# Optimization experiments

Measured on AMD Instinct MI355X. Metric: run time of the kernel, lower is better.

Reference implementation:

```python
import jax, jax.numpy as jnp
import numpy as np

EPS = 1e-30
NEG = -1e30  # finite stand-in for -inf (safe under vjp, exp underflows to 0)


def _build_tree(L):
    """Perfect binary tree with L leaves (L power of 2) plus a unifurcating root.
    Node ids are level-contiguous (leaves first), which is a valid postorder-compatible
    numbering for the level-synchronous pruning loop."""
    depth = int(np.log2(L))
    total = 2 * L  # (2L-1) perfect-tree nodes + 1 unifurcating root
    children = np.full((total, 2), -1, dtype=np.int64)
    parents = np.full(total, -1, dtype=np.int64)
    levels = np.zeros(total, dtype=np.int64)
    offs = np.zeros(depth + 1, dtype=np.int64)
    for h in range(1, depth + 1):
        offs[h] = offs[h - 1] + (L >> (h - 1))
    for h in range(1, depth + 1):
        n = L >> h
        ids = offs[h] + np.arange(n)
        lkid = offs[h - 1] + 2 * np.arange(n)
        children[ids, 0] = lkid
        children[ids, 1] = lkid + 1
        parents[lkid] = ids
        parents[lkid + 1] = ids
        levels[ids] = h
    root = total - 1
    top = offs[depth]  # the single node at level `depth`
    children[root, 0] = top  # unifurcating root: right child = -1
    parents[top] = root
    levels[root] = depth + 1
    return children, parents, levels


def setup_inputs() -> dict:
    key = jax.random.key(0)
    S = 16
    L = 32768  # leaves -> N = 65536 nodes
    children, parents, levels = _build_tree(L)
    N = children.shape[0]
    postorder = np.arange(N, dtype=np.int64)
    k1, k2, k3, k4 = jax.random.split(key, 4)
    branch_lens = jax.random.uniform(k1, (N,), jnp.float32, 0.05, 0.5)
    branch_lens = branch_lens.at[N - 1].set(0.0)  # root edge has length 0
    # CTMC-style rate matrix: nonneg off-diagonals, rows sum to 0
    off = jax.random.uniform(k2, (S, S), jnp.float32, 0.1, 1.0) * (1.0 - jnp.eye(S, dtype=jnp.float32))
    Q = off - jnp.diag(off.sum(axis=1))
    growth_rates = jax.random.uniform(k3, (S,), jnp.float32, 0.5, 1.5)
    leaf_states = np.asarray(jax.random.randint(k4, (L,), 0, S))
    init_partials = np.full((N, S), NEG, dtype=np.float32)
    init_partials[np.arange(L), leaf_states] = 0.0  # leaf one-hots in log space
    return {
        "postorder": jnp.asarray(postorder),
        "children": jnp.asarray(children),
        "parents": jnp.asarray(parents),
        "branch_lens": branch_lens,
        "init_partials": jnp.asarray(init_partials),
        "Q": Q,
        "levels": jnp.asarray(levels),
        "growth_rates": growth_rates,
    }


def _log_prune(branch_lens, init_partials, Q, growth_rates, po, ch, lv):
    S = Q.shape[0]
    # rho == 1.0 path of FelsensteinPruner.log_prune
    rate = Q - jnp.diag(growth_rates)
    scaled = rate[None, :, :] * branch_lens[:, None, None]      # (N, S, S)
    trans = jax.vmap(jax.scipy.linalg.expm)(scaled)             # batched matrix_exp
    I = jnp.eye(S, dtype=Q.dtype)
    trans = jnp.where((branch_lens <= EPS)[:, None, None], I[None], trans)
    log_trans = jnp.log(jnp.clip(trans, EPS))
    log_growth = jnp.log(growth_rates)
    log_partials = init_partials
    max_level = int(lv.max())
    for lvl in range(1, max_level + 1):  # tree topology is static -> static level groups
        node_idxs = po[lv == lvl]
        left = ch[node_idxs, 0]
        right = ch[node_idxs, 1]
        # left_contrib[n, p] = logsumexp_c( log P_left[n, p, c] + L_left[n, c] )
        lc = jax.nn.logsumexp(log_trans[left] + log_partials[left][:, None, :], axis=2)
        valid = np.nonzero(right >= 0)[0]
        rc = jnp.zeros_like(lc)
        if valid.size > 0:
            rv = right[valid]
            rc_v = jax.nn.logsumexp(log_trans[rv] + log_partials[rv][:, None, :], axis=2)
            rc_v = rc_v + log_growth[None, :]  # growth_rates term on the right child
            rc = rc.at[valid].set(rc_v)
        log_partials = log_partials.at[node_idxs].set(lc + rc)
    root = int(po[lv == max_level][0])
    return log_partials[root]


def reference(postorder, children, parents, branch_lens, init_partials, Q, levels, growth_rates):
    po = np.asarray(postorder)
    ch = np.asarray(children)
    lv = np.asarray(levels)
    return _log_prune(branch_lens, init_partials, Q, growth_rates, po, ch, lv)
```

## Files before the change

### kernel.cpp

```cpp
#include <hip/hip_runtime.h>
#include <math.h>

#define KORD 10
#define NC   (KORD + 1)
#define NTOT 65536
#define MAGIC 0x5A17C0DEu

typedef float f32x2 __attribute__((ext_vector_type(2)));

static constexpr int WS_U6  = 0;
static constexpr int WS_S6  = 8192;
static constexpr int WS_U11 = 8704;
static constexpr int WS_S11 = 8960;
static constexpr int WS_F1  = 8976;
static constexpr int WS_F2  = 9488;


template <int CTRL>
__device__ __forceinline__ float qperm_add(float x) {
  const int xi = __builtin_bit_cast(int, x);
  const int yi = __builtin_amdgcn_mov_dpp(xi, CTRL, 0xF, 0xF, true);
  return x + __builtin_bit_cast(float, yi);
}

__device__ __forceinline__ float horner_dot(const f32x2* c01, const f32x2* c23,
                                            float tv, float4 uu) {
  const f32x2 t2 = {tv, tv};
  f32x2 a01 = c01[KORD], a23 = c23[KORD];
  #pragma unroll
  for (int k = KORD - 1; k >= 0; --k) {
    a01 = __builtin_elementwise_fma(a01, t2, c01[k]);
    a23 = __builtin_elementwise_fma(a23, t2, c23[k]);
  }
  const f32x2 u01 = {uu.x, uu.y}, u23 = {uu.z, uu.w};
  f32x2 mm = a01 * u01;
  mm = __builtin_elementwise_fma(a23, u23, mm);
  float yy = mm.x + mm.y;
  yy = qperm_add<0xB1>(yy);
  yy = qperm_add<0x4E>(yy);
  return yy;
}

__device__ __forceinline__ int tree_sweep(
    float* ubuf, float* sbuf, const float* blB,
    const f32x2* c01, const f32x2* c23, float sigma, float gp,
    int IN, int depth, int t)
{
  const int lane = t & 63;
  const int wid = t >> 6;
  const int p = (lane >> 2) & 15;
  const int q = lane & 3;
  int off_in = 0, bloff = 0;
  for (int ll = 1; ll <= depth; ++ll) {
    const int cnt = IN >> ll;
    const int off_out = off_in + (IN >> (ll - 1));
    for (int n = wid; n < cnt; n += 8) {
      const int cl = 2 * n, cr = cl + 1;
      const float tl = blB[bloff + cl];
      const float tr = blB[bloff + cr];
      const float4 uL = *(const float4*)&ubuf[(off_in + cl) * 16 + q * 4];
      const float4 uR = *(const float4*)&ubuf[(off_in + cr) * 16 + q * 4];
      const float yl = horner_dot(c01, c23, tl, uL);
      const float yr = horner_dot(c01, c23, tr, uR);
      const float val = yl * yr * gp;
      const float mx = __shfl(val, 28 + q, 64);
      const float un = val * __builtin_amdgcn_rcpf(mx);
      if (q == 0) ubuf[(off_out + n) * 16 + p] = un;
      if (lane == 0)
        sbuf[off_out + n] = sbuf[off_in + cl] + sbuf[off_in + cr] +
                            sigma * (tl + tr) + __logf(mx);
    }
    bloff += IN >> (ll - 1);
    off_in = off_out;
    __syncthreads();
  }
  return off_in;
}

__device__ __forceinline__ void stage_bl(float* blB, const float* bl,
                                         int b, int IN, int depth,
                                         int level_in, int tt) {
  int loff = 0;
  for (int ll = 1; ll <= depth; ++ll) {
    const int cnt_c = IN >> (ll - 1);
    const int gl = level_in + ll - 1;
    const int cbase = (gl == 0) ? 0 : (NTOT - (NTOT >> gl));
    if (tt < cnt_c) blB[loff + tt] = bl[cbase + b * cnt_c + tt];
    loff += cnt_c;
  }
}

__device__ __forceinline__ void poll_reset(unsigned int* f) {
  while (__hip_atomic_load(f, __ATOMIC_RELAXED, __HIP_MEMORY_SCOPE_AGENT)
         != MAGIC)
    __builtin_amdgcn_s_sleep(1);
  __hip_atomic_store(f, 0u, __ATOMIC_RELAXED, __HIP_MEMORY_SCOPE_AGENT);
}

__device__ __forceinline__ float row_dot16(const float4* row, const float* col) {
  const float4 r0 = row[0], r1 = row[1], r2 = row[2], r3 = row[3];
  float s = r0.x * col[0];
  s = fmaf(r0.y, col[1], s);  s = fmaf(r0.z, col[2], s);
  s = fmaf(r0.w, col[3], s);  s = fmaf(r1.x, col[4], s);
  s = fmaf(r1.y, col[5], s);  s = fmaf(r1.z, col[6], s);
  s = fmaf(r1.w, col[7], s);  s = fmaf(r2.x, col[8], s);
  s = fmaf(r2.y, col[9], s);  s = fmaf(r2.z, col[10], s);
  s = fmaf(r2.w, col[11], s); s = fmaf(r3.x, col[12], s);
  s = fmaf(r3.y, col[13], s); s = fmaf(r3.z, col[14], s);
  s = fmaf(r3.w, col[15], s);
  return s;
}

__global__ __launch_bounds__(512) void k_all(
    const float* __restrict__ bl, const float* __restrict__ init_p,
    const float* __restrict__ Q, const float* __restrict__ g,
    float* __restrict__ ws, float* __restrict__ out)
{
  __shared__ __align__(16) float Bs[256];
  __shared__ __align__(16) float BsT[256];
  __shared__ __align__(16) float B2T[256];
  __shared__ __align__(16) float Cs[NC * 256];
  __shared__ __align__(16) float ubuf[127 * 16];
  __shared__ float sbuf[127];
  __shared__ float blB[128];
  __shared__ float sdiag[16];
  __shared__ float s_sig;

  const int t = threadIdx.x, b = blockIdx.x;
  const int lane = t & 63, wid = t >> 6;
  const int p = (lane >> 2) & 15, q = lane & 3;
  const int i = (t & 255) >> 4, j = t & 15;
  unsigned int* f1 = (unsigned int*)(ws + WS_F1);
  unsigned int* f2 = (unsigned int*)(ws + WS_F2);

  float4 leafv;
  float blr[6];
  const int tt = t - 256;
  if (t >= 256) {
    leafv = ((const float4*)init_p)[b * 256 + tt];
    int cnt_c = 64, base = 0;
    #pragma unroll
    for (int ll = 1; ll <= 6; ++ll) {
      if (tt < cnt_c) blr[ll - 1] = bl[base + b * cnt_c + tt];
      base = NTOT - (NTOT >> ll);
      cnt_c >>= 1;
    }
  }

  float a = 0.0f;
  if (t < 256) {
    a = Q[t] - ((i == j) ? g[i] : 0.0f);
    if (i == j) sdiag[i] = a;
  }
  __syncthreads();
  if (t == 0) {
    float m = sdiag[0];
    for (int r = 1; r < 16; ++r) m = fminf(m, sdiag[r]);
    s_sig = m;
  }
  __syncthreads();
  const float sigma = s_sig;
  if (t < 256) {
    const float bv = a - ((i == j) ? sigma : 0.0f);
    Bs[t] = bv;
    BsT[j * 16 + i] = bv;
    Cs[t] = (i == j) ? 1.0f : 0.0f;
    Cs[256 + t] = bv;
  }
  __syncthreads();
  if (t < 256) {
    float bcol[16];
    #pragma unroll
    for (int c = 0; c < 4; ++c)
      *(float4*)&bcol[c * 4] = *(const float4*)&BsT[j * 16 + c * 4];
    const float s = row_dot16((const float4*)&Bs[i * 16], bcol);
    B2T[j * 16 + i] = s;
  }
  __syncthreads();
  float b2col[16];
  #pragma unroll
  for (int c = 0; c < 4; ++c)
    *(float4*)&b2col[c * 4] = *(const float4*)&B2T[j * 16 + c * 4];
  #pragma unroll
  for (int m = 0; m < 5; ++m) {
    if (t < 256) {
      const float s = row_dot16((const float4*)&Cs[(2 * m) * 256 + i * 16], b2col);
      Cs[(2 * m + 2) * 256 + t] = s * (1.0f / (float)((2 * m + 1) * (2 * m + 2)));
    } else if (m < 4) {
      const float s = row_dot16((const float4*)&Cs[(2 * m + 1) * 256 + i * 16], b2col);
      Cs[(2 * m + 3) * 256 + (t - 256)] =
          s * (1.0f / (float)((2 * m + 2) * (2 * m + 3)));
    }
    __syncthreads();
  }
  f32x2 c01[NC], c23[NC];
  #pragma unroll
  for (int k = 0; k <= KORD; ++k) {
    const float4 v = *(const float4*)&Cs[k * 256 + p * 16 + q * 4];
    c01[k] = f32x2{v.x, v.y};
    c23[k] = f32x2{v.z, v.w};
  }
  const float gp = g[p];

  if (t >= 256) {
    float4 v = leafv;
    v.x = (v.x > -0.5f) ? 1.0f : 0.0f;
    v.y = (v.y > -0.5f) ? 1.0f : 0.0f;
    v.z = (v.z > -0.5f) ? 1.0f : 0.0f;
    v.w = (v.w > -0.5f) ? 1.0f : 0.0f;
    ((float4*)ubuf)[tt] = v;
    if (tt < 64) sbuf[tt] = 0.0f;
    int loff = 0, cnt_c = 64;
    #pragma unroll
    for (int ll = 1; ll <= 6; ++ll) {
      if (tt < cnt_c) blB[loff + tt] = blr[ll - 1];
      loff += cnt_c;
      cnt_c >>= 1;
    }
  }
  __syncthreads();

  {
    const int off = tree_sweep(ubuf, sbuf, blB, c01, c23, sigma, gp, 64, 6, t);
    if (t < 16)
      __hip_atomic_store(&ws[WS_U6 + b * 16 + t], ubuf[off * 16 + t],
                         __ATOMIC_RELAXED, __HIP_MEMORY_SCOPE_AGENT);
    if (t == 16)
      __hip_atomic_store(&ws[WS_S6 + b], sbuf[off],
                         __ATOMIC_RELAXED, __HIP_MEMORY_SCOPE_AGENT);
    asm volatile("s_waitcnt vmcnt(0)" ::: "memory");
    if (t == 0)
      __hip_atomic_store(&f1[b], MAGIC,
                         __ATOMIC_RELAXED, __HIP_MEMORY_SCOPE_AGENT);
  }
  if (b >= 16) return;

  if (t < 32) poll_reset(&f1[b * 32 + t]);
  __syncthreads();
  if (t < 32 * 16)
    ubuf[t] = __hip_atomic_load(&ws[WS_U6 + b * 512 + t], __ATOMIC_RELAXED,
                                __HIP_MEMORY_SCOPE_AGENT);
  if (t < 32)
    sbuf[t] = __hip_atomic_load(&ws[WS_S6 + b * 32 + t], __ATOMIC_RELAXED,
                                __HIP_MEMORY_SCOPE_AGENT);
  if (t >= 256) stage_bl(blB, bl, b, 32, 5, 6, t - 256);
  __syncthreads();
  {
    const int off = tree_sweep(ubuf, sbuf, blB, c01, c23, sigma, gp, 32, 5, t);
    if (t < 16)
      __hip_atomic_store(&ws[WS_U11 + b * 16 + t], ubuf[off * 16 + t],
                         __ATOMIC_RELAXED, __HIP_MEMORY_SCOPE_AGENT);
    if (t == 16)
      __hip_atomic_store(&ws[WS_S11 + b], sbuf[off],
                         __ATOMIC_RELAXED, __HIP_MEMORY_SCOPE_AGENT);
    asm volatile("s_waitcnt vmcnt(0)" ::: "memory");
    if (t == 0)
      __hip_atomic_store(&f2[b], MAGIC,
                         __ATOMIC_RELAXED, __HIP_MEMORY_SCOPE_AGENT);
  }
  if (b > 0) return;

  if (t < 16) poll_reset(&f2[t]);
  __syncthreads();
  if (t < 16 * 16)
    ubuf[t] = __hip_atomic_load(&ws[WS_U11 + t], __ATOMIC_RELAXED,
                                __HIP_MEMORY_SCOPE_AGENT);
  if (t < 16)
    sbuf[t] = __hip_atomic_load(&ws[WS_S11 + t], __ATOMIC_RELAXED,
                                __HIP_MEMORY_SCOPE_AGENT);
  if (t >= 256) stage_bl(blB, bl, 0, 16, 4, 11, t - 256);
  __syncthreads();
  {
    const int off = tree_sweep(ubuf, sbuf, blB, c01, c23, sigma, gp, 16, 4, t);
    if (wid == 0) {
      const float tr = bl[NTOT - 2];
      const float4 u = *(const float4*)&ubuf[off * 16 + q * 4];
      const float y = horner_dot(c01, c23, tr, u);
      if (q == 0) out[p] = logf(y) + sbuf[off] + sigma * tr;
    }
  }
}

extern "C" void kernel_launch(void* const* d_in, const int* in_sizes, int n_in,
                              void* d_out, int out_size, void* d_ws, size_t ws_size,
                              hipStream_t stream) {
  const float* bl     = (const float*)d_in[3];
  const float* init_p = (const float*)d_in[4];
  const float* Q      = (const float*)d_in[5];
  const float* growth = (const float*)d_in[7];
  float* ws  = (float*)d_ws;
  float* out = (float*)d_out;

  k_all<<<512, 512, 0, stream>>>(bl, init_p, Q, growth, ws, out);
}
```

Baseline: 23.58 us.

## Halve block count with 128-leaf subtrees and move combiners to last blocks

```diff
diff --git a/kernel.cpp b/kernel.cpp
--- a/kernel.cpp
+++ b/kernel.cpp
@@ -5,15 +5,17 @@
 #define NC   (KORD + 1)
 #define NTOT 65536
 #define MAGIC 0x5A17C0DEu
+#define NB   256
+#define CB0  240
 
 typedef float f32x2 __attribute__((ext_vector_type(2)));
 
-static constexpr int WS_U6  = 0;
-static constexpr int WS_S6  = 8192;
-static constexpr int WS_U11 = 8704;
-static constexpr int WS_S11 = 8960;
-static constexpr int WS_F1  = 8976;
-static constexpr int WS_F2  = 9488;
+static constexpr int WS_U7  = 0;
+static constexpr int WS_S7  = 4096;
+static constexpr int WS_U11 = 4352;
+static constexpr int WS_S11 = 4608;
+static constexpr int WS_F1  = 4624;
+static constexpr int WS_F2  = 4880;
 
 
 template <int CTRL>
@@ -78,14 +80,14 @@
 }
 
 __device__ __forceinline__ void stage_bl(float* blB, const float* bl,
-                                         int b, int IN, int depth,
+                                         int grp, int IN, int depth,
                                          int level_in, int tt) {
   int loff = 0;
   for (int ll = 1; ll <= depth; ++ll) {
     const int cnt_c = IN >> (ll - 1);
     const int gl = level_in + ll - 1;
     const int cbase = (gl == 0) ? 0 : (NTOT - (NTOT >> gl));
-    if (tt < cnt_c) blB[loff + tt] = bl[cbase + b * cnt_c + tt];
+    if (tt < cnt_c) blB[loff + tt] = bl[cbase + grp * cnt_c + tt];
     loff += cnt_c;
   }
 }
@@ -120,9 +122,9 @@
   __shared__ __align__(16) float BsT[256];
   __shared__ __align__(16) float B2T[256];
   __shared__ __align__(16) float Cs[NC * 256];
-  __shared__ __align__(16) float ubuf[127 * 16];
-  __shared__ float sbuf[127];
-  __shared__ float blB[128];
+  __shared__ __align__(16) float ubuf[255 * 16];
+  __shared__ float sbuf[255];
+  __shared__ float blB[254];
   __shared__ float sdiag[16];
   __shared__ float s_sig;
 
@@ -130,20 +132,19 @@
   const int lane = t & 63, wid = t >> 6;
   const int p = (lane >> 2) & 15, q = lane & 3;
   const int i = (t & 255) >> 4, j = t & 15;
+  const int tt = t - 256;
   unsigned int* f1 = (unsigned int*)(ws + WS_F1);
   unsigned int* f2 = (unsigned int*)(ws + WS_F2);
 
-  float4 leafv;
-  float blr[6];
-  const int tt = t - 256;
+  float4 leafv = ((const float4*)init_p)[b * 512 + t];
+  float blr[7];
   if (t >= 256) {
-    leafv = ((const float4*)init_p)[b * 256 + tt];
-    int cnt_c = 64, base = 0;
+    int cnt = 128, base = 0;
     #pragma unroll
-    for (int ll = 1; ll <= 6; ++ll) {
-      if (tt < cnt_c) blr[ll - 1] = bl[base + b * cnt_c + tt];
+    for (int ll = 1; ll <= 7; ++ll) {
+      if (tt < cnt) blr[ll - 1] = bl[base + b * cnt + tt];
       base = NTOT - (NTOT >> ll);
-      cnt_c >>= 1;
+      cnt >>= 1;
     }
   }
 
@@ -188,7 +189,7 @@
       Cs[(2 * m + 2) * 256 + t] = s * (1.0f / (float)((2 * m + 1) * (2 * m + 2)));
     } else if (m < 4) {
       const float s = row_dot16((const float4*)&Cs[(2 * m + 1) * 256 + i * 16], b2col);
-      Cs[(2 * m + 3) * 256 + (t - 256)] =
+      Cs[(2 * m + 3) * 256 + tt] =
           s * (1.0f / (float)((2 * m + 2) * (2 * m + 3)));
     }
     __syncthreads();
@@ -202,73 +203,76 @@
   }
   const float gp = g[p];
 
-  if (t >= 256) {
+  {
     float4 v = leafv;
     v.x = (v.x > -0.5f) ? 1.0f : 0.0f;
     v.y = (v.y > -0.5f) ? 1.0f : 0.0f;
     v.z = (v.z > -0.5f) ? 1.0f : 0.0f;
     v.w = (v.w > -0.5f) ? 1.0f : 0.0f;
-    ((float4*)ubuf)[tt] = v;
-    if (tt < 64) sbuf[tt] = 0.0f;
-    int loff = 0, cnt_c = 64;
+    ((float4*)ubuf)[t] = v;
+  }
+  if (t < 128) sbuf[t] = 0.0f;
+  if (t >= 256) {
+    int loff = 0, cnt = 128;
     #pragma unroll
-    for (int ll = 1; ll <= 6; ++ll) {
-      if (tt < cnt_c) blB[loff + tt] = blr[ll - 1];
-      loff += cnt_c;
-      cnt_c >>= 1;
-    }
-  }
-  __syncthreads();
-
-  {
-    const int off = tree_sweep(ubuf, sbuf, blB, c01, c23, sigma, gp, 64, 6, t);
+    for (int ll = 1; ll <= 7; ++ll) {
+      if (tt < cnt) blB[loff + tt] = blr[ll - 1];
+      loff += cnt;
+      cnt >>= 1;
+    }
+  }
+  __syncthreads();
+
+  {
+    const int off = tree_sweep(ubuf, sbuf, blB, c01, c23, sigma, gp, 128, 7, t);
     if (t < 16)
-      __hip_atomic_store(&ws[WS_U6 + b * 16 + t], ubuf[off * 16 + t],
+      __hip_atomic_store(&ws[WS_U7 + b * 16 + t], ubuf[off * 16 + t],
                          __ATOMIC_RELAXED, __HIP_MEMORY_SCOPE_AGENT);
     if (t == 16)
-      __hip_atomic_store(&ws[WS_S6 + b], sbuf[off],
+      __hip_atomic_store(&ws[WS_S7 + b], sbuf[off],
                          __ATOMIC_RELAXED, __HIP_MEMORY_SCOPE_AGENT);
     asm volatile("s_waitcnt vmcnt(0)" ::: "memory");
     if (t == 0)
       __hip_atomic_store(&f1[b], MAGIC,
                          __ATOMIC_RELAXED, __HIP_MEMORY_SCOPE_AGENT);
   }
-  if (b >= 16) return;
-
-  if (t < 32) poll_reset(&f1[b * 32 + t]);
-  __syncthreads();
-  if (t < 32 * 16)
-    ubuf[t] = __hip_atomic_load(&ws[WS_U6 + b * 512 + t], __ATOMIC_RELAXED,
-                                __HIP_MEMORY_SCOPE_AGENT);
-  if (t < 32)
-    sbuf[t] = __hip_atomic_load(&ws[WS_S6 + b * 32 + t], __ATOMIC_RELAXED,
-                                __HIP_MEMORY_SCOPE_AGENT);
-  if (t >= 256) stage_bl(blB, bl, b, 32, 5, 6, t - 256);
-  __syncthreads();
-  {
-    const int off = tree_sweep(ubuf, sbuf, blB, c01, c23, sigma, gp, 32, 5, t);
+  if (b < CB0) return;
+  const int c = b - CB0;
+
+  if (t < 16) poll_reset(&f1[c * 16 + t]);
+  __syncthreads();
+  if (t < 256)
+    ubuf[t] = __hip_atomic_load(&ws[WS_U7 + c * 256 + t], __ATOMIC_RELAXED,
+                                __HIP_MEMORY_SCOPE_AGENT);
+  if (t < 16)
+    sbuf[t] = __hip_atomic_load(&ws[WS_S7 + c * 16 + t], __ATOMIC_RELAXED,
+                                __HIP_MEMORY_SCOPE_AGENT);
+  if (t >= 256) stage_bl(blB, bl, c, 16, 4, 7, tt);
+  __syncthreads();
+  {
+    const int off = tree_sweep(ubuf, sbuf, blB, c01, c23, sigma, gp, 16, 4, t);
     if (t < 16)
-      __hip_atomic_store(&ws[WS_U11 + b * 16 + t], ubuf[off * 16 + t],
+      __hip_atomic_store(&ws[WS_U11 + c * 16 + t], ubuf[off * 16 + t],
                          __ATOMIC_RELAXED, __HIP_MEMORY_SCOPE_AGENT);
     if (t == 16)
-      __hip_atomic_store(&ws[WS_S11 + b], sbuf[off],
+      __hip_atomic_store(&ws[WS_S11 + c], sbuf[off],
                          __ATOMIC_RELAXED, __HIP_MEMORY_SCOPE_AGENT);
     asm volatile("s_waitcnt vmcnt(0)" ::: "memory");
     if (t == 0)
-      __hip_atomic_store(&f2[b], MAGIC,
-                         __ATOMIC_RELAXED, __HIP_MEMORY_SCOPE_AGENT);
-  }
-  if (b > 0) return;
+      __hip_atomic_store(&f2[c], MAGIC,
+                         __ATOMIC_RELAXED, __HIP_MEMORY_SCOPE_AGENT);
+  }
+  if (b != NB - 1) return;
 
   if (t < 16) poll_reset(&f2[t]);
   __syncthreads();
-  if (t < 16 * 16)
+  if (t < 256)
     ubuf[t] = __hip_atomic_load(&ws[WS_U11 + t], __ATOMIC_RELAXED,
                                 __HIP_MEMORY_SCOPE_AGENT);
   if (t < 16)
     sbuf[t] = __hip_atomic_load(&ws[WS_S11 + t], __ATOMIC_RELAXED,
                                 __HIP_MEMORY_SCOPE_AGENT);
-  if (t >= 256) stage_bl(blB, bl, 0, 16, 4, 11, t - 256);
+  if (t >= 256) stage_bl(blB, bl, 0, 16, 4, 11, tt);
   __syncthreads();
   {
     const int off = tree_sweep(ubuf, sbuf, blB, c01, c23, sigma, gp, 16, 4, t);
@@ -291,5 +295,5 @@
   float* ws  = (float*)d_ws;
   float* out = (float*)d_out;
 
-  k_all<<<512, 512, 0, stream>>>(bl, init_p, Q, growth, ws, out);
-}
+  k_all<<<NB, 512, 0, stream>>>(bl, init_p, Q, growth, ws, out);
+}
```

Measured after the change: 23.84 us. About the same (+1.1%).
